# Kernel tuning notes

Hardware: AMD Instinct MI355X
Metric: run time of the kernel (lower is better)

## Reference

```python
import jax, jax.numpy as jnp
import numpy as np

N = 16384        # total atoms
E = 262144       # edges
D = 128          # dim_embedding
F = 128          # num_filters
G = 50           # num_gaussians
L = 4            # num_interactions
CUTOFF = 5.0
GAMMA = 4.0
NUM_MOLS = 32
LOG2 = float(np.log(2.0))


def ssp(x):
    # ShiftedSoftplus: softplus(x) - log(2)
    return jax.nn.softplus(x) - LOG2


def setup_inputs() -> dict:
    key = jax.random.key(0)
    ks = jax.random.split(key, 24)
    s = lambda *sh: 1.0 / np.sqrt(sh[-2]) if len(sh) >= 2 else 0.1
    inp = {
        "z": jax.random.normal(ks[0], (N, 1), jnp.float32),
        "pos": jax.random.uniform(ks[1], (N, 3), jnp.float32),
        "batch": jnp.sort(jax.random.randint(ks[2], (N,), 0, NUM_MOLS)),
        "edge_src": jax.random.randint(ks[3], (E,), 0, N),
        "edge_dst": jax.random.randint(ks[4], (E,), 0, N),
        # embedding Linear(1, D)
        "emb_W": jax.random.normal(ks[5], (1, D), jnp.float32),
        "emb_b": jax.random.normal(ks[6], (D,), jnp.float32) * 0.1,
        # per-interaction stacked params [L, ...]
        "mlp_W1": jax.random.normal(ks[7], (L, G, F), jnp.float32) / np.sqrt(G),
        "mlp_b1": jnp.zeros((L, F), jnp.float32),
        "mlp_W2": jax.random.normal(ks[8], (L, F, F), jnp.float32) / np.sqrt(F),
        "mlp_b2": jnp.zeros((L, F), jnp.float32),
        "cf1_W": jax.random.normal(ks[9], (L, D, F), jnp.float32) / np.sqrt(D),   # CFConv.lin1 (no bias)
        "cf2_W": jax.random.normal(ks[10], (L, F, D), jnp.float32) / np.sqrt(F),  # CFConv.lin2
        "cf2_b": jnp.zeros((L, D), jnp.float32),
        "int_lin_W": jax.random.normal(ks[11], (L, D, D), jnp.float32) / np.sqrt(D),
        "int_lin_b": jnp.zeros((L, D), jnp.float32),
        # readout head
        "lin1_W": jax.random.normal(ks[12], (D, D // 2), jnp.float32) / np.sqrt(D),
        "lin1_b": jnp.zeros((D // 2,), jnp.float32),
        "lin2_W": jax.random.normal(ks[13], (D // 2, 1), jnp.float32) / np.sqrt(D // 2),
        "lin2_b": jnp.zeros((1,), jnp.float32),
    }
    return inp


def reference(z, pos, batch, edge_src, edge_dst, emb_W, emb_b,
              mlp_W1, mlp_b1, mlp_W2, mlp_b2, cf1_W, cf2_W, cf2_b,
              int_lin_W, int_lin_b, lin1_W, lin1_b, lin2_W, lin2_b):
    # atom embedding: Linear(1, D)
    h = z @ emb_W + emb_b                                  # [N, D]

    # interaction graph distances (graph connectivity precomputed)
    diff = pos[edge_src] - pos[edge_dst]                   # [E, 3]
    dist = jnp.sqrt(jnp.sum(diff * diff, axis=-1) + 1e-12) # [E]

    # radial basis expansion
    mu = jnp.linspace(0.0, CUTOFF, G).astype(h.dtype)      # [G]
    rbf = jnp.exp(-GAMMA * (dist[:, None] - mu) ** 2)      # [E, G]

    # cosine cutoff envelope
    C = 0.5 * (jnp.cos(dist * (np.pi / CUTOFF)) + 1.0)     # [E]

    for l in range(L):
        # continuous filter from RBF: MLP [E,G] -> [E,F]
        Wf = ssp(rbf @ mlp_W1[l] + mlp_b1[l]) @ mlp_W2[l] + mlp_b2[l]
        Wf = Wf * C[:, None]                               # [E, F]
        # CFConv: gather - multiply - scatter-add
        xj = (h @ cf1_W[l])[edge_src]                      # [E, F]
        agg = jax.ops.segment_sum(xj * Wf, edge_dst, num_segments=N)  # [N, F]
        x = agg @ cf2_W[l] + cf2_b[l]                      # [N, D]
        x = ssp(x)
        x = x @ int_lin_W[l] + int_lin_b[l]
        h = h + x                                          # residual

    h = ssp(h @ lin1_W + lin1_b) @ lin2_W + lin2_b         # [N, 1]
    out = jax.ops.segment_sum(h, batch, num_segments=NUM_MOLS)  # [NUM_MOLS, 1]
    return out
```

## Files before the change

### kernel.cpp

```cpp
#include <hip/hip_runtime.h>
#include <hip/hip_bf16.h>
#include <math.h>

#define N_ATOMS 16384
#define N_EDGES 262144
#define DIM 128
#define NF 128
#define NG 50
#define NL 4
#define NMOLS 32
#define EW 8
#define EB 4

typedef short bf16x8 __attribute__((ext_vector_type(8)));
typedef float f32x4 __attribute__((ext_vector_type(4)));

__device__ __forceinline__ float ssp_f(float x) {
    float e = __expf(-fabsf(x));
    return fmaxf(x, 0.0f) + __logf(1.0f + e) - 0.6931471805599453f;
}

__device__ __forceinline__ short f2bf(float x) {
    __hip_bfloat16 b = __float2bfloat16(x);
    return *reinterpret_cast<short*>(&b);
}

__device__ __forceinline__ float bf2f(unsigned short u) {
    unsigned int v = ((unsigned int)u) << 16;
    return __builtin_bit_cast(float, v);
}

__global__ void k_embed(const float* __restrict__ z, const float* __restrict__ Wv,
                        const float* __restrict__ bv, float* __restrict__ h) {
    int idx = blockIdx.x * blockDim.x + threadIdx.x;
    int n = idx >> 7, d = idx & 127;
    h[idx] = z[n] * Wv[d] + bv[d];
}

__global__ void k_geom(const float* __restrict__ pos, const int* __restrict__ src,
                       const int* __restrict__ dst, float* __restrict__ dist,
                       float* __restrict__ Cenv) {
    int e = blockIdx.x * blockDim.x + threadIdx.x;
    if (e >= N_EDGES) return;
    int s = src[e], t = dst[e];
    float dx = pos[3*s]   - pos[3*t];
    float dy = pos[3*s+1] - pos[3*t+1];
    float dz = pos[3*s+2] - pos[3*t+2];
    float d = sqrtf(dx*dx + dy*dy + dz*dz + 1e-12f);
    dist[e] = d;
    Cenv[e] = 0.5f * (cosf(d * (float)(M_PI / 5.0)) + 1.0f);
}

__global__ void k_deg(const int* __restrict__ dst, int* __restrict__ deg) {
    int e = blockIdx.x * blockDim.x + threadIdx.x;
    if (e < N_EDGES) atomicAdd(&deg[dst[e]], 1);
}

__global__ __launch_bounds__(1024)
void k_scan(const int* __restrict__ deg, int* __restrict__ cur) {
    __shared__ int tot[1024];
    int t = threadIdx.x;
    int v[16];
    int s = 0;
    #pragma unroll
    for (int j = 0; j < 16; ++j) { int x = deg[t * 16 + j]; v[j] = s; s += x; }
    tot[t] = s;
    __syncthreads();
    for (int off = 1; off < 1024; off <<= 1) {
        int add = (t >= off) ? tot[t - off] : 0;
        __syncthreads();
        tot[t] += add;
        __syncthreads();
    }
    int base = (t == 0) ? 0 : tot[t - 1];
    #pragma unroll
    for (int j = 0; j < 16; ++j) cur[t * 16 + j] = base + v[j];
}

__global__ void k_fill(const int* __restrict__ dst, int* __restrict__ cur,
                       int* __restrict__ edge_of) {
    int e = blockIdx.x * blockDim.x + threadIdx.x;
    if (e < N_EDGES) {
        int p = atomicAdd(&cur[dst[e]], 1);
        edge_of[p] = e;
    }
}

__global__ void k_perm(const int* __restrict__ edge_of, const float* __restrict__ dist,
                       const float* __restrict__ Cenv, const int* __restrict__ src,
                       const int* __restrict__ dst, float* __restrict__ distS,
                       float* __restrict__ CenvS, int* __restrict__ srcS,
                       int* __restrict__ dstS) {
    int p = blockIdx.x * blockDim.x + threadIdx.x;
    if (p >= N_EDGES) return;
    int e = edge_of[p];
    distS[p] = dist[e];
    CenvS[p] = Cenv[e];
    srcS[p]  = src[e];
    dstS[p]  = dst[e];
}

__global__ __launch_bounds__(512)
void k_rbf(const float* __restrict__ distS, short* __restrict__ rbfF) {
    int lane = threadIdx.x & 63;
    int w    = threadIdx.x >> 6;
    int t    = blockIdx.x * 8 + w;
    int q = lane >> 4, m = lane & 15;
    float d = distS[t * 16 + m];
    #pragma unroll
    for (int kc = 0; kc < 2; ++kc) {
        bf16x8 v;
        #pragma unroll
        for (int j = 0; j < 8; ++j) {
            float mu = (float)(kc * 32 + q * 8 + j) * (5.0f / 49.0f);
            float tt = d - mu;
            v[j] = f2bf(__expf(-4.0f * tt * tt));
        }
        *(bf16x8*)&rbfF[(size_t)((t * 2 + kc) * 64 + lane) * 8] = v;
    }
}

__global__ __launch_bounds__(512, 4)
void k_edge_csr(const short* __restrict__ rbfF, const float* __restrict__ CenvS,
                const int* __restrict__ srcS, const int* __restrict__ dstS,
                const float* __restrict__ W1, const float* __restrict__ b1,
                const float* __restrict__ W2, const float* __restrict__ b2,
                const unsigned short* __restrict__ xjb, float* __restrict__ agg)
{
    __shared__ short H1s[64 * 128];
    __shared__ unsigned short msgt[64][136];
    __shared__ int dsts[64];
    __shared__ unsigned long long maskS;
    const int tid  = threadIdx.x;
    const int lane = tid & 63;
    const int w    = tid >> 6;
    const int q    = lane >> 4;
    const int m    = lane & 15;

    bf16x8 W1R[2], W2R[4];
    #pragma unroll
    for (int kc = 0; kc < 2; ++kc) {
        bf16x8 f;
        #pragma unroll
        for (int j = 0; j < 8; ++j) {
            int k = kc * 32 + q * 8 + j;
            float v = (k < NG) ? W1[k * NF + w * 16 + m] : 0.0f;
            f[j] = f2bf(v);
        }
        W1R[kc] = f;
    }
    #pragma unroll
    for (int kc = 0; kc < 4; ++kc) {
        bf16x8 f;
        #pragma unroll
        for (int j = 0; j < 8; ++j) {
            int k = kc * 32 + q * 8 + j;
            f[j] = f2bf(W2[k * NF + w * 16 + m]);
        }
        W2R[kc] = f;
    }
    const float b1v = b1[w * 16 + m];
    const float b2v = b2[w * 16 + m];

    const int nrounds = N_EDGES / 64;
    for (int r = blockIdx.x; r < nrounds; r += gridDim.x) {
        const int p0 = r * 64;
        short* H = H1s;

        #pragma unroll
        for (int a = 0; a < 4; ++a) {
            int tile = r * 4 + a;
            f32x4 acc = {b1v, b1v, b1v, b1v};
            #pragma unroll
            for (int kc = 0; kc < 2; ++kc) {
                bf16x8 A = *(const bf16x8*)&rbfF[(size_t)((tile * 2 + kc) * 64 + lane) * 8];
                acc = __builtin_amdgcn_mfma_f32_16x16x32_bf16(A, W1R[kc], acc, 0, 0, 0);
            }
            #pragma unroll
            for (int i = 0; i < 4; ++i) {
                int e = a * 16 + q * 4 + i;
                int f = w * 16 + m;
                int byte = (e * 256 + f * 2) ^ ((e & 7) << 4);
                *(short*)((char*)H + byte) = f2bf(ssp_f(acc[i]));
            }
        }
        __syncthreads();

        unsigned short xu[4][4];
        #pragma unroll
        for (int a = 0; a < 4; ++a) {
            int4 s4 = *(const int4*)&srcS[p0 + a * 16 + q * 4];
            #pragma unroll
            for (int i = 0; i < 4; ++i)
                xu[a][i] = xjb[(size_t)((const int*)&s4)[i] * NF + w * 16 + m];
        }

        f32x4 acc2[4];
        #pragma unroll
        for (int a = 0; a < 4; ++a) {
            f32x4 acc = {b2v, b2v, b2v, b2v};
            #pragma unroll
            for (int kc = 0; kc < 4; ++kc) {
                int e = a * 16 + m;
                int byte = (e * 256 + (kc * 32 + q * 8) * 2) ^ ((e & 7) << 4);
                bf16x8 A = *(const bf16x8*)((const char*)H + byte);
                acc = __builtin_amdgcn_mfma_f32_16x16x32_bf16(A, W2R[kc], acc, 0, 0, 0);
            }
            acc2[a] = acc;
        }

        #pragma unroll
        for (int a = 0; a < 4; ++a) {
            float4 cc4 = *(const float4*)&CenvS[p0 + a * 16 + q * 4];
            #pragma unroll
            for (int i = 0; i < 4; ++i) {
                float v = acc2[a][i] * ((const float*)&cc4)[i];
                msgt[a * 16 + q * 4 + i][w * 16 + m] =
                    (unsigned short)f2bf(v * bf2f(xu[a][i]));
            }
        }
        if (w == 0) {
            int d = dstS[p0 + lane];
            int prev = __shfl_up(d, 1);
            bool head = (lane == 0) || (d != prev);
            unsigned long long mk = __ballot(head);
            dsts[lane] = d;
            if (lane == 0) maskS = mk;
        }
        __syncthreads();

        {
            int f = tid & 127;
            int g = tid >> 7;
            unsigned long long mm = maskS;
            int k = 0;
            while (mm) {
                int start = __ffsll(mm) - 1;
                mm &= mm - 1;
                int end = mm ? (__ffsll(mm) - 1) : 64;
                if ((k & 3) == g) {
                    float s0 = 0.0f, s1 = 0.0f, s2 = 0.0f, s3 = 0.0f;
                    int p = start;
                    for (; p + 4 <= end; p += 4) {
                        s0 += bf2f(msgt[p    ][f]);
                        s1 += bf2f(msgt[p + 1][f]);
                        s2 += bf2f(msgt[p + 2][f]);
                        s3 += bf2f(msgt[p + 3][f]);
                    }
                    for (; p < end; ++p) s0 += bf2f(msgt[p][f]);
                    float s = (s0 + s1) + (s2 + s3);
                    float* addr = &agg[(size_t)dsts[start] * NF + f];
                    if (start == 0 || end == 64) atomicAdd(addr, s);
                    else *addr = s;
                }
                ++k;
            }
        }
    }
}

template<int ACT, int RESID, int OUTBF>
__global__ __launch_bounds__(512, 2)
void k_node_mfma(const float* __restrict__ in, const float* __restrict__ W,
                 const float* __restrict__ bias, const float* __restrict__ resid,
                 void* __restrict__ outv)
{
    __shared__ short T[32 * 128];
    const int tid  = threadIdx.x;
    const int lane = tid & 63;
    const int w    = tid >> 6;
    const int q    = lane >> 4;
    const int m    = lane & 15;

    bf16x8 WR[4];
    #pragma unroll
    for (int kc = 0; kc < 4; ++kc) {
        bf16x8 f;
        #pragma unroll
        for (int j = 0; j < 8; ++j)
            f[j] = f2bf(W[(kc * 32 + q * 8 + j) * DIM + w * 16 + m]);
        WR[kc] = f;
    }
    const float bv = bias ? bias[w * 16 + m] : 0.0f;

    const int r0 = blockIdx.x * 32;

    {
        int row = tid >> 4;
        int k0  = (tid & 15) * 8;
        const float* src = in + (size_t)(r0 + row) * DIM + k0;
        float4 v0 = *(const float4*)(src);
        float4 v1 = *(const float4*)(src + 4);
        bf16x8 lo;
        #pragma unroll
        for (int j = 0; j < 4; ++j) {
            lo[j]     = f2bf(((const float*)&v0)[j]);
            lo[j + 4] = f2bf(((const float*)&v1)[j]);
        }
        int b0 = (row * 256 + k0 * 2) ^ ((row & 7) << 4);
        *(bf16x8*)((char*)T + b0) = lo;
    }
    __syncthreads();

    #pragma unroll
    for (int a = 0; a < 2; ++a) {
        f32x4 acc = {bv, bv, bv, bv};
        int row = a * 16 + m;
        #pragma unroll
        for (int kc = 0; kc < 4; ++kc) {
            int byte = (row * 256 + (kc * 32 + q * 8) * 2) ^ ((row & 7) << 4);
            bf16x8 A = *(const bf16x8*)((const char*)T + byte);
            acc = __builtin_amdgcn_mfma_f32_16x16x32_bf16(A, WR[kc], acc, 0, 0, 0);
        }
        #pragma unroll
        for (int i = 0; i < 4; ++i) {
            float v = acc[i];
            if (ACT) v = ssp_f(v);
            size_t oi = (size_t)(r0 + a * 16 + q * 4 + i) * DIM + w * 16 + m;
            if (RESID) v += resid[oi];
            if (OUTBF) ((unsigned short*)outv)[oi] = (unsigned short)f2bf(v);
            else       ((float*)outv)[oi] = v;
        }
    }
}

__global__ __launch_bounds__(512, 2)
void k_node_fused(const float* __restrict__ agg, const float* __restrict__ W2,
                  const float* __restrict__ b2, const float* __restrict__ Wi,
                  const float* __restrict__ bi, float* __restrict__ h)
{
    __shared__ short T[32 * 128];
    __shared__ short X[32 * 128];
    const int tid  = threadIdx.x;
    const int lane = tid & 63;
    const int w    = tid >> 6;
    const int q    = lane >> 4;
    const int m    = lane & 15;

    bf16x8 W2R[4], WiR[4];
    #pragma unroll
    for (int kc = 0; kc < 4; ++kc) {
        bf16x8 f2v, fiv;
        #pragma unroll
        for (int j = 0; j < 8; ++j) {
            int k = kc * 32 + q * 8 + j;
            f2v[j] = f2bf(W2[k * DIM + w * 16 + m]);
            fiv[j] = f2bf(Wi[k * DIM + w * 16 + m]);
        }
        W2R[kc] = f2v;
        WiR[kc] = fiv;
    }
    const float b2v = b2[w * 16 + m];
    const float biv = bi[w * 16 + m];

    const int r0 = blockIdx.x * 32;

    {
        int row = tid >> 4;
        int k0  = (tid & 15) * 8;
        const float* src = agg + (size_t)(r0 + row) * DIM + k0;
        float4 v0 = *(const float4*)(src);
        float4 v1 = *(const float4*)(src + 4);
        bf16x8 lo;
        #pragma unroll
        for (int j = 0; j < 4; ++j) {
            lo[j]     = f2bf(((const float*)&v0)[j]);
            lo[j + 4] = f2bf(((const float*)&v1)[j]);
        }
        int b0 = (row * 256 + k0 * 2) ^ ((row & 7) << 4);
        *(bf16x8*)((char*)T + b0) = lo;
    }
    __syncthreads();

    #pragma unroll
    for (int a = 0; a < 2; ++a) {
        f32x4 acc = {b2v, b2v, b2v, b2v};
        int row = a * 16 + m;
        #pragma unroll
        for (int kc = 0; kc < 4; ++kc) {
            int byte = (row * 256 + (kc * 32 + q * 8) * 2) ^ ((row & 7) << 4);
            bf16x8 A = *(const bf16x8*)((const char*)T + byte);
            acc = __builtin_amdgcn_mfma_f32_16x16x32_bf16(A, W2R[kc], acc, 0, 0, 0);
        }
        #pragma unroll
        for (int i = 0; i < 4; ++i) {
            int orow = a * 16 + q * 4 + i;
            int ocol = w * 16 + m;
            int byte = (orow * 256 + ocol * 2) ^ ((orow & 7) << 4);
            *(short*)((char*)X + byte) = f2bf(ssp_f(acc[i]));
        }
    }
    __syncthreads();

    #pragma unroll
    for (int a = 0; a < 2; ++a) {
        f32x4 acc = {biv, biv, biv, biv};
        int row = a * 16 + m;
        #pragma unroll
        for (int kc = 0; kc < 4; ++kc) {
            int byte = (row * 256 + (kc * 32 + q * 8) * 2) ^ ((row & 7) << 4);
            bf16x8 A = *(const bf16x8*)((const char*)X + byte);
            acc = __builtin_amdgcn_mfma_f32_16x16x32_bf16(A, WiR[kc], acc, 0, 0, 0);
        }
        #pragma unroll
        for (int i = 0; i < 4; ++i) {
            size_t oi = (size_t)(r0 + a * 16 + q * 4 + i) * DIM + w * 16 + m;
            h[oi] += acc[i];
        }
    }
}

template<int COLS, int ACT, int RESID>
__global__ __launch_bounds__(512)
void k_node_gemm(const float* __restrict__ in, const float* __restrict__ W,
                 const float* __restrict__ bias, const float* __restrict__ resid,
                 float* __restrict__ out)
{
    __shared__ float Ws[DIM][COLS];
    __shared__ float rs[EW][EB][DIM];
    int tid = threadIdx.x;
    for (int i = tid; i < DIM * COLS; i += 512) (&Ws[0][0])[i] = W[i];
    __syncthreads();

    int lane = tid & 63;
    int w = tid >> 6;
    int gw = blockIdx.x * EW + w;
    int nw = gridDim.x * EW;
    int ngroups = N_ATOMS / EB;
    constexpr int CPL = COLS / 64;

    float bb[CPL];
    #pragma unroll
    for (int c = 0; c < CPL; ++c) bb[c] = bias ? bias[lane + 64 * c] : 0.0f;

    for (int grp = gw; grp < ngroups; grp += nw) {
        int r0 = grp * EB;
        #pragma unroll
        for (int r = 0; r < EB; ++r) {
            rs[w][r][lane]      = in[(size_t)(r0 + r) * DIM + lane];
            rs[w][r][lane + 64] = in[(size_t)(r0 + r) * DIM + lane + 64];
        }
        float acc[EB][CPL];
        #pragma unroll
        for (int r = 0; r < EB; ++r)
            #pragma unroll
            for (int c = 0; c < CPL; ++c) acc[r][c] = bb[c];
        #pragma unroll 2
        for (int kb = 0; kb < DIM / 4; ++kb) {
            float4 rv[EB];
            #pragma unroll
            for (int r = 0; r < EB; ++r)
                rv[r] = *(const float4*)&rs[w][r][4 * kb];
            #pragma unroll
            for (int j = 0; j < 4; ++j) {
                float wv[CPL];
                #pragma unroll
                for (int c = 0; c < CPL; ++c) wv[c] = Ws[4 * kb + j][lane + 64 * c];
                #pragma unroll
                for (int r = 0; r < EB; ++r) {
                    float rj = ((const float*)&rv[r])[j];
                    #pragma unroll
                    for (int c = 0; c < CPL; ++c)
                        acc[r][c] = fmaf(rj, wv[c], acc[r][c]);
                }
            }
        }
        #pragma unroll
        for (int r = 0; r < EB; ++r) {
            #pragma unroll
            for (int c = 0; c < CPL; ++c) {
                float v = acc[r][c];
                if (ACT) v = ssp_f(v);
                size_t oi = (size_t)(r0 + r) * COLS + lane + 64 * c;
                if (RESID) v += resid[oi];
                out[oi] = v;
            }
        }
    }
}

__global__ __launch_bounds__(256)
void k_final(const float* __restrict__ r1, const float* __restrict__ l2W,
             const float* __restrict__ l2b, const int* __restrict__ batch,
             float* __restrict__ out)
{
    __shared__ float mols[NMOLS];
    int tid = threadIdx.x;
    if (tid < NMOLS) mols[tid] = 0.0f;
    __syncthreads();

    int n = blockIdx.x * 256 + tid;
    const float4* row = (const float4*)(r1 + (size_t)n * 64);
    const float4* wv  = (const float4*)l2W;
    float s = 0.0f;
    #pragma unroll
    for (int k = 0; k < 16; ++k) {
        float4 a = row[k], b = wv[k];
        s += a.x * b.x + a.y * b.y + a.z * b.z + a.w * b.w;
    }
    s += l2b[0];
    atomicAdd(&mols[batch[n]], s);
    __syncthreads();
    if (tid < NMOLS) atomicAdd(&out[tid], mols[tid]);
}

extern "C" void kernel_launch(void* const* d_in, const int* in_sizes, int n_in,
                              void* d_out, int out_size, void* d_ws, size_t ws_size,
                              hipStream_t stream) {
    const float* z     = (const float*)d_in[0];
    const float* pos   = (const float*)d_in[1];
    const int*   batch = (const int*)d_in[2];
    const int*   esrc  = (const int*)d_in[3];
    const int*   edst  = (const int*)d_in[4];
    const float* embW  = (const float*)d_in[5];
    const float* embB  = (const float*)d_in[6];
    const float* mlpW1 = (const float*)d_in[7];
    const float* mlpB1 = (const float*)d_in[8];
    const float* mlpW2 = (const float*)d_in[9];
    const float* mlpB2 = (const float*)d_in[10];
    const float* cf1W  = (const float*)d_in[11];
    const float* cf2W  = (const float*)d_in[12];
    const float* cf2B  = (const float*)d_in[13];
    const float* intW  = (const float*)d_in[14];
    const float* intB  = (const float*)d_in[15];
    const float* l1W   = (const float*)d_in[16];
    const float* l1B   = (const float*)d_in[17];
    const float* l2W   = (const float*)d_in[18];
    const float* l2B   = (const float*)d_in[19];
    float* out = (float*)d_out;

    char* ws = (char*)d_ws;
    float* h     = (float*)(ws);
    float* dist  = (float*)(ws + (size_t)( 8 << 20));
    float* Cv    = (float*)(ws + (size_t)( 9 << 20));
    unsigned short* xj = (unsigned short*)(ws + (size_t)(10 << 20));
    float* agg   = (float*)(ws + (size_t)(18 << 20));
    short* rbfF  = (short*)(ws + (size_t)(26 << 20));
    int*   deg   = (int*)  (ws + (size_t)(58 << 20));
    int*   cur   = (int*)  (ws + (size_t)(59 << 20));
    int*   edge_of = (int*)(ws + (size_t)(60 << 20));
    float* distS = (float*)(ws + (size_t)(61 << 20));
    float* CenvS = (float*)(ws + (size_t)(62 << 20));
    int*   srcS  = (int*)  (ws + (size_t)(63 << 20));
    int*   dstS  = (int*)  (ws + (size_t)(64 << 20));
    float* r1    = agg;

    k_embed<<<dim3(N_ATOMS * DIM / 512), dim3(512), 0, stream>>>(z, embW, embB, h);
    k_geom<<<dim3(N_EDGES / 256), dim3(256), 0, stream>>>(pos, esrc, edst, dist, Cv);

    hipMemsetAsync(deg, 0, N_ATOMS * sizeof(int), stream);
    k_deg<<<dim3(N_EDGES / 512), dim3(512), 0, stream>>>(edst, deg);
    k_scan<<<dim3(1), dim3(1024), 0, stream>>>(deg, cur);
    k_fill<<<dim3(N_EDGES / 512), dim3(512), 0, stream>>>(edst, cur, edge_of);
    k_perm<<<dim3(N_EDGES / 512), dim3(512), 0, stream>>>(edge_of, dist, Cv, esrc, edst,
                                                          distS, CenvS, srcS, dstS);
    k_rbf<<<dim3(N_EDGES / 16 / 8), dim3(512), 0, stream>>>(distS, rbfF);

    for (int l = 0; l < NL; ++l) {
        k_node_mfma<0, 0, 1><<<dim3(N_ATOMS / 32), dim3(512), 0, stream>>>(
            h, cf1W + (size_t)l * DIM * NF, nullptr, nullptr, (void*)xj);
        hipMemsetAsync(agg, 0, (size_t)N_ATOMS * NF * sizeof(float), stream);
        k_edge_csr<<<dim3(1024), dim3(512), 0, stream>>>(
            rbfF, CenvS, srcS, dstS,
            mlpW1 + (size_t)l * NG * NF, mlpB1 + (size_t)l * NF,
            mlpW2 + (size_t)l * NF * NF, mlpB2 + (size_t)l * NF,
            xj, agg);
        k_node_fused<<<dim3(N_ATOMS / 32), dim3(512), 0, stream>>>(
            agg, cf2W + (size_t)l * NF * DIM, cf2B + (size_t)l * DIM,
            intW + (size_t)l * DIM * DIM, intB + (size_t)l * DIM, h);
    }

    k_node_gemm<64, 1, 0><<<dim3(256), dim3(512), 0, stream>>>(h, l1W, l1B, nullptr, r1);
    hipMemsetAsync(out, 0, NMOLS * sizeof(float), stream);
    k_final<<<dim3(N_ATOMS / 256), dim3(256), 0, stream>>>(r1, l2W, l2B, batch, out);
}
```

Measured before the change: 482.8 us.

## Fuse next-layer lin1 projection and agg zeroing into node kernel

The embed and geometry kernels are merged into one launch. The node-update kernel now also computes the next layer's cf1 projection from the freshly updated h held in shared memory, writes xj as bf16, and zeroes agg for the next edge pass. This replaces the per-layer k_node_mfma launch and the memset. It removes several launches and one full read of h per layer, at the cost of more register pressure from a third weight fragment set and an extra barrier.

```diff
diff --git a/kernel.cpp b/kernel.cpp
--- a/kernel.cpp
+++ b/kernel.cpp
@@ -30,25 +30,25 @@
     return __builtin_bit_cast(float, v);
 }
 
-__global__ void k_embed(const float* __restrict__ z, const float* __restrict__ Wv,
-                        const float* __restrict__ bv, float* __restrict__ h) {
-    int idx = blockIdx.x * blockDim.x + threadIdx.x;
+__global__ __launch_bounds__(512)
+void k_embed_geom(const float* __restrict__ z, const float* __restrict__ Wv,
+                  const float* __restrict__ bv, float* __restrict__ h,
+                  const float* __restrict__ pos, const int* __restrict__ src,
+                  const int* __restrict__ dst, float* __restrict__ dist,
+                  float* __restrict__ Cenv) {
+    int idx = blockIdx.x * 512 + threadIdx.x;
     int n = idx >> 7, d = idx & 127;
     h[idx] = z[n] * Wv[d] + bv[d];
-}
-
-__global__ void k_geom(const float* __restrict__ pos, const int* __restrict__ src,
-                       const int* __restrict__ dst, float* __restrict__ dist,
-                       float* __restrict__ Cenv) {
-    int e = blockIdx.x * blockDim.x + threadIdx.x;
-    if (e >= N_EDGES) return;
-    int s = src[e], t = dst[e];
-    float dx = pos[3*s]   - pos[3*t];
-    float dy = pos[3*s+1] - pos[3*t+1];
-    float dz = pos[3*s+2] - pos[3*t+2];
-    float d = sqrtf(dx*dx + dy*dy + dz*dz + 1e-12f);
-    dist[e] = d;
-    Cenv[e] = 0.5f * (cosf(d * (float)(M_PI / 5.0)) + 1.0f);
+    if (blockIdx.x < N_EDGES / 512) {
+        int e = blockIdx.x * 512 + threadIdx.x;
+        int s = src[e], t = dst[e];
+        float dx = pos[3*s]   - pos[3*t];
+        float dy = pos[3*s+1] - pos[3*t+1];
+        float dz = pos[3*s+2] - pos[3*t+2];
+        float dd = sqrtf(dx*dx + dy*dy + dz*dz + 1e-12f);
+        dist[e] = dd;
+        Cenv[e] = 0.5f * (cosf(dd * (float)(M_PI / 5.0)) + 1.0f);
+    }
 }
 
 __global__ void k_deg(const int* __restrict__ dst, int* __restrict__ deg) {
@@ -263,7 +263,7 @@
 __global__ __launch_bounds__(512, 2)
 void k_node_mfma(const float* __restrict__ in, const float* __restrict__ W,
                  const float* __restrict__ bias, const float* __restrict__ resid,
-                 void* __restrict__ outv)
+                 void* __restrict__ outv, float* __restrict__ aggz)
 {
     __shared__ short T[32 * 128];
     const int tid  = threadIdx.x;
@@ -299,6 +299,12 @@
         }
         int b0 = (row * 256 + k0 * 2) ^ ((row & 7) << 4);
         *(bf16x8*)((char*)T + b0) = lo;
+        if (aggz) {
+            float4 zz = {0.0f, 0.0f, 0.0f, 0.0f};
+            float* dz = aggz + (size_t)(r0 + row) * DIM + k0;
+            *(float4*)dz = zz;
+            *(float4*)(dz + 4) = zz;
+        }
     }
     __syncthreads();
 
@@ -324,10 +330,13 @@
     }
 }
 
+template<int EMIT>
 __global__ __launch_bounds__(512, 2)
 void k_node_fused(const float* __restrict__ agg, const float* __restrict__ W2,
                   const float* __restrict__ b2, const float* __restrict__ Wi,
-                  const float* __restrict__ bi, float* __restrict__ h)
+                  const float* __restrict__ bi, float* __restrict__ h,
+                  const float* __restrict__ W1n, unsigned short* __restrict__ xjn,
+                  float* __restrict__ aggz)
 {
     __shared__ short T[32 * 128];
     __shared__ short X[32 * 128];
@@ -337,7 +346,7 @@
     const int q    = lane >> 4;
     const int m    = lane & 15;
 
-    bf16x8 W2R[4], WiR[4];
+    bf16x8 W2R[4], WiR[4], W1nR[4];
     #pragma unroll
     for (int kc = 0; kc < 4; ++kc) {
         bf16x8 f2v, fiv;
@@ -350,15 +359,25 @@
         W2R[kc] = f2v;
         WiR[kc] = fiv;
     }
+    if constexpr (EMIT) {
+        #pragma unroll
+        for (int kc = 0; kc < 4; ++kc) {
+            bf16x8 f;
+            #pragma unroll
+            for (int j = 0; j < 8; ++j)
+                f[j] = f2bf(W1n[(kc * 32 + q * 8 + j) * DIM + w * 16 + m]);
+            W1nR[kc] = f;
+        }
+    }
     const float b2v = b2[w * 16 + m];
     const float biv = bi[w * 16 + m];
 
     const int r0 = blockIdx.x * 32;
+    const int srow = tid >> 4;
+    const int sk0  = (tid & 15) * 8;
 
     {
-        int row = tid >> 4;
-        int k0  = (tid & 15) * 8;
-        const float* src = agg + (size_t)(r0 + row) * DIM + k0;
+        const float* src = agg + (size_t)(r0 + srow) * DIM + sk0;
         float4 v0 = *(const float4*)(src);
         float4 v1 = *(const float4*)(src + 4);
         bf16x8 lo;
@@ -367,7 +386,7 @@
             lo[j]     = f2bf(((const float*)&v0)[j]);
             lo[j + 4] = f2bf(((const float*)&v1)[j]);
         }
-        int b0 = (row * 256 + k0 * 2) ^ ((row & 7) << 4);
+        int b0 = (srow * 256 + sk0 * 2) ^ ((srow & 7) << 4);
         *(bf16x8*)((char*)T + b0) = lo;
     }
     __syncthreads();
@@ -405,7 +424,41 @@
         #pragma unroll
         for (int i = 0; i < 4; ++i) {
             size_t oi = (size_t)(r0 + a * 16 + q * 4 + i) * DIM + w * 16 + m;
-            h[oi] += acc[i];
+            float v = h[oi] + acc[i];
+            h[oi] = v;
+            if constexpr (EMIT) {
+                int orow = a * 16 + q * 4 + i;
+                int ocol = w * 16 + m;
+                int byte = (orow * 256 + ocol * 2) ^ ((orow & 7) << 4);
+                *(short*)((char*)T + byte) = f2bf(v);
+            }
+        }
+    }
+
+    if constexpr (EMIT) {
+        {
+            float4 zz = {0.0f, 0.0f, 0.0f, 0.0f};
+            float* dz = aggz + (size_t)(r0 + srow) * DIM + sk0;
+            *(float4*)dz = zz;
+            *(float4*)(dz + 4) = zz;
+        }
+        __syncthreads();
+
+        #pragma unroll
+        for (int a = 0; a < 2; ++a) {
+            f32x4 acc = {0.0f, 0.0f, 0.0f, 0.0f};
+            int row = a * 16 + m;
+            #pragma unroll
+            for (int kc = 0; kc < 4; ++kc) {
+                int byte = (row * 256 + (kc * 32 + q * 8) * 2) ^ ((row & 7) << 4);
+                bf16x8 A = *(const bf16x8*)((const char*)T + byte);
+                acc = __builtin_amdgcn_mfma_f32_16x16x32_bf16(A, W1nR[kc], acc, 0, 0, 0);
+            }
+            #pragma unroll
+            for (int i = 0; i < 4; ++i) {
+                size_t oi = (size_t)(r0 + a * 16 + q * 4 + i) * DIM + w * 16 + m;
+                xjn[oi] = (unsigned short)f2bf(acc[i]);
+            }
         }
     }
 }
@@ -545,8 +598,8 @@
     int*   dstS  = (int*)  (ws + (size_t)(64 << 20));
     float* r1    = agg;
 
-    k_embed<<<dim3(N_ATOMS * DIM / 512), dim3(512), 0, stream>>>(z, embW, embB, h);
-    k_geom<<<dim3(N_EDGES / 256), dim3(256), 0, stream>>>(pos, esrc, edst, dist, Cv);
+    k_embed_geom<<<dim3(N_ATOMS * DIM / 512), dim3(512), 0, stream>>>(
+        z, embW, embB, h, pos, esrc, edst, dist, Cv);
 
     hipMemsetAsync(deg, 0, N_ATOMS * sizeof(int), stream);
     k_deg<<<dim3(N_EDGES / 512), dim3(512), 0, stream>>>(edst, deg);
@@ -556,18 +609,26 @@
                                                           distS, CenvS, srcS, dstS);
     k_rbf<<<dim3(N_EDGES / 16 / 8), dim3(512), 0, stream>>>(distS, rbfF);
 
+    k_node_mfma<0, 0, 1><<<dim3(N_ATOMS / 32), dim3(512), 0, stream>>>(
+        h, cf1W, nullptr, nullptr, (void*)xj, agg);
+
     for (int l = 0; l < NL; ++l) {
-        k_node_mfma<0, 0, 1><<<dim3(N_ATOMS / 32), dim3(512), 0, stream>>>(
-            h, cf1W + (size_t)l * DIM * NF, nullptr, nullptr, (void*)xj);
-        hipMemsetAsync(agg, 0, (size_t)N_ATOMS * NF * sizeof(float), stream);
         k_edge_csr<<<dim3(1024), dim3(512), 0, stream>>>(
             rbfF, CenvS, srcS, dstS,
             mlpW1 + (size_t)l * NG * NF, mlpB1 + (size_t)l * NF,
             mlpW2 + (size_t)l * NF * NF, mlpB2 + (size_t)l * NF,
             xj, agg);
-        k_node_fused<<<dim3(N_ATOMS / 32), dim3(512), 0, stream>>>(
-            agg, cf2W + (size_t)l * NF * DIM, cf2B + (size_t)l * DIM,
-            intW + (size_t)l * DIM * DIM, intB + (size_t)l * DIM, h);
+        if (l < NL - 1) {
+            k_node_fused<1><<<dim3(N_ATOMS / 32), dim3(512), 0, stream>>>(
+                agg, cf2W + (size_t)l * NF * DIM, cf2B + (size_t)l * DIM,
+                intW + (size_t)l * DIM * DIM, intB + (size_t)l * DIM, h,
+                cf1W + (size_t)(l + 1) * DIM * NF, xj, agg);
+        } else {
+            k_node_fused<0><<<dim3(N_ATOMS / 32), dim3(512), 0, stream>>>(
+                agg, cf2W + (size_t)l * NF * DIM, cf2B + (size_t)l * DIM,
+                intW + (size_t)l * DIM * DIM, intB + (size_t)l * DIM, h,
+                nullptr, nullptr, nullptr);
+        }
     }
 
     k_node_gemm<64, 1, 0><<<dim3(256), dim3(512), 0, stream>>>(h, l1W, l1B, nullptr, r1);
```

Measured after the change: 463.6 us. -4.0%, faster.
